# Kernel optimization log

Measured on AMD Instinct MI355X. Metric: run time of the kernel, lower is better.

The kernel has to match this reference:

```python
import jax, jax.numpy as jnp
import numpy as np

NUM_HEADS = 16
WINDOW = 256
DIM = 1024


def setup_inputs() -> dict:
    key = jax.random.key(0)
    k1, k2, k3, k4, k5 = jax.random.split(key, 5)
    B, L, D = 2, 2048, DIM
    s = 1.0 / np.sqrt(D)
    return {
        "x": jax.random.normal(k1, (B, L, D), dtype=jnp.float32),
        "in_proj_w": jax.random.uniform(k2, (3 * D, D), dtype=jnp.float32, minval=-s, maxval=s),
        "in_proj_b": jax.random.uniform(k3, (3 * D,), dtype=jnp.float32, minval=-s, maxval=s),
        "out_w": jax.random.uniform(k4, (D, D), dtype=jnp.float32, minval=-s, maxval=s),
        "out_b": jax.random.uniform(k5, (D,), dtype=jnp.float32, minval=-s, maxval=s),
    }


def reference(x, in_proj_w, in_proj_b, out_w, out_b):
    B, L, D = x.shape
    H = NUM_HEADS
    hd = D // H

    # combined qkv projection, as in nn.MultiheadAttention
    qkv = x @ in_proj_w.T + in_proj_b          # [B, L, 3D]
    q, k, v = jnp.split(qkv, 3, axis=-1)
    q = q.reshape(B, L, H, hd).transpose(0, 2, 1, 3)  # [B, H, L, hd]
    k = k.reshape(B, L, H, hd).transpose(0, 2, 1, 3)
    v = v.reshape(B, L, H, hd).transpose(0, 2, 1, 3)

    scale = 1.0 / jnp.sqrt(jnp.asarray(hd, dtype=x.dtype))
    scores = jnp.einsum("bhqd,bhkd->bhqk", q * scale, k)  # [B, H, L, L]

    # sliding-window causal mask: allowed iff i-window < j <= i
    i = jnp.arange(L)[:, None]
    j = jnp.arange(L)[None, :]
    allowed = (j <= i) & (j > i - WINDOW)                  # [L, L]
    scores = jnp.where(allowed[None, None], scores, -jnp.inf)

    attn = jax.nn.softmax(scores, axis=-1)
    out = jnp.einsum("bhqk,bhkd->bhqd", attn, v)           # [B, H, L, hd]
    out = out.transpose(0, 2, 1, 3).reshape(B, L, D)
    return out @ out_w.T + out_b
```

## Files before the change

### kernel.cpp

```cpp
#include <hip/hip_runtime.h>


#define SEQ_L 2048
#define WIN   256

typedef __bf16 bf16x8 __attribute__((ext_vector_type(8)));
typedef float  f32x4  __attribute__((ext_vector_type(4)));

__device__ __forceinline__ unsigned short f32_to_bf16(float f) {
  unsigned int u = __float_as_uint(f);
  u += 0x7FFFu + ((u >> 16) & 1u);
  return (unsigned short)(u >> 16);
}

__global__ void cast_kernel(const float* __restrict__ in,
                            unsigned short* __restrict__ out, int n4) {
  int i = blockIdx.x * 256 + threadIdx.x;
  if (i >= n4) return;
  float4 v = ((const float4*)in)[i];
  ushort4 o;
  o.x = f32_to_bf16(v.x); o.y = f32_to_bf16(v.y);
  o.z = f32_to_bf16(v.z); o.w = f32_to_bf16(v.w);
  ((ushort4*)out)[i] = o;
}

#define BK  64
#define LDK 72

template<int TBM, int TBN, int MI, int NI, int OUTBF>
__global__ __launch_bounds__(256) void gemm_nt(
    const unsigned short* __restrict__ A,
    const unsigned short* __restrict__ Bt,
    const float* __restrict__ bias,
    void* __restrict__ Cout, int M, int N, int K)
{
  __shared__ unsigned short As[TBM * LDK];
  __shared__ unsigned short Bs[TBN * LDK];

  const int tid  = threadIdx.x;
  const int lane = tid & 63;
  const int wave = tid >> 6;
  const int wr   = (wave >> 1) * (MI * 16);
  const int wc   = (wave & 1) * (NI * 16);
  const int quad = lane >> 4;
  const int l16  = lane & 15;

  const long m0 = (long)blockIdx.y * TBM;
  const long n0 = (long)blockIdx.x * TBN;

  f32x4 acc[MI][NI];
#pragma unroll
  for (int i = 0; i < MI; ++i)
#pragma unroll
    for (int j = 0; j < NI; ++j)
#pragma unroll
      for (int r = 0; r < 4; ++r) acc[i][j][r] = 0.0f;

  for (int k0 = 0; k0 < K; k0 += BK) {
#pragma unroll
    for (int p = 0; p < TBM / 32; ++p) {
      int c = p * 256 + tid, row = c >> 3, col8 = c & 7;
      *(uint4*)(&As[row * LDK + col8 * 8]) =
          *(const uint4*)(A + (m0 + row) * (long)K + k0 + col8 * 8);
    }
#pragma unroll
    for (int p = 0; p < TBN / 32; ++p) {
      int c = p * 256 + tid, row = c >> 3, col8 = c & 7;
      *(uint4*)(&Bs[row * LDK + col8 * 8]) =
          *(const uint4*)(Bt + (n0 + row) * (long)K + k0 + col8 * 8);
    }
    __syncthreads();
#pragma unroll
    for (int ks = 0; ks < 2; ++ks) {
      bf16x8 af[MI], bfv[NI];
#pragma unroll
      for (int mi = 0; mi < MI; ++mi)
        af[mi] = *(const bf16x8*)(&As[(wr + mi * 16 + l16) * LDK + ks * 32 + quad * 8]);
#pragma unroll
      for (int ni = 0; ni < NI; ++ni)
        bfv[ni] = *(const bf16x8*)(&Bs[(wc + ni * 16 + l16) * LDK + ks * 32 + quad * 8]);
#pragma unroll
      for (int mi = 0; mi < MI; ++mi)
#pragma unroll
        for (int ni = 0; ni < NI; ++ni)
          acc[mi][ni] = __builtin_amdgcn_mfma_f32_16x16x32_bf16(af[mi], bfv[ni], acc[mi][ni], 0, 0, 0);
    }
    __syncthreads();
  }

#pragma unroll
  for (int ni = 0; ni < NI; ++ni) {
    long col = n0 + wc + ni * 16 + l16;
    float bv = bias[col];
#pragma unroll
    for (int mi = 0; mi < MI; ++mi) {
      long rowb = m0 + wr + mi * 16 + quad * 4;
#pragma unroll
      for (int r = 0; r < 4; ++r) {
        float v = acc[mi][ni][r] + bv;
        if (OUTBF) ((unsigned short*)Cout)[(rowb + r) * N + col] = f32_to_bf16(v);
        else       ((float*)Cout)[(rowb + r) * N + col] = v;
      }
    }
  }
}

__global__ __launch_bounds__(256) void attn_kernel(
    const unsigned short* __restrict__ qkv,
    unsigned short* __restrict__ aout)
{
  __shared__ unsigned short Ks[64 * 72];
  __shared__ unsigned short Vt[64 * 72];
  __shared__ unsigned short Ps[4 * 16 * 72];

  const int tid  = threadIdx.x;
  const int w    = tid >> 6;
  const int lane = tid & 63;
  const int quad = lane >> 4;
  const int l16  = lane & 15;

  const int blk = blockIdx.x;
  const int qt  = blk & 31;
  const int h   = (blk >> 5) & 15;
  const int b   = blk >> 9;

  const int  i0  = qt * 64;
  const int  i0w = i0 + w * 16;
  const long rowbase = (long)b * SEQ_L;
  const float NEG_INF = -__builtin_inff();

  bf16x8 aq[2];
  {
    const unsigned short* qp = qkv + (rowbase + i0w + l16) * 3072 + h * 64 + quad * 8;
    aq[0] = *(const bf16x8*)(qp);
    aq[1] = *(const bf16x8*)(qp + 32);
  }

  f32x4 o[4];
#pragma unroll
  for (int ni = 0; ni < 4; ++ni)
#pragma unroll
    for (int r = 0; r < 4; ++r) o[ni][r] = 0.0f;
  float m_i[4], l_i[4];
#pragma unroll
  for (int r = 0; r < 4; ++r) { m_i[r] = NEG_INF; l_i[r] = 0.0f; }

  unsigned short* psw = &Ps[w * 16 * 72];

  const int j_begin = (i0 >= WIN) ? i0 - WIN : 0;

  for (int j0 = j_begin; j0 <= i0; j0 += 64) {
    __syncthreads();
#pragma unroll
    for (int p = 0; p < 2; ++p) {
      int c = p * 256 + tid, row = c >> 3, col8 = c & 7;
      const unsigned short* base = qkv + (rowbase + j0 + row) * 3072 + h * 64 + col8 * 8;
      *(uint4*)(&Ks[row * 72 + col8 * 8]) = *(const uint4*)(base + 1024);
      unsigned short tmp[8];
      *(uint4*)tmp = *(const uint4*)(base + 2048);
      int rsw = row ^ (col8 << 3);
#pragma unroll
      for (int e = 0; e < 8; ++e)
        Vt[(col8 * 8 + e) * 72 + rsw] = tmp[e];
    }
    __syncthreads();

    f32x4 s[4];
#pragma unroll
    for (int g = 0; g < 4; ++g) {
      bf16x8 k0 = *(const bf16x8*)(&Ks[(g * 16 + l16) * 72 + quad * 8]);
      bf16x8 k1 = *(const bf16x8*)(&Ks[(g * 16 + l16) * 72 + 32 + quad * 8]);
      f32x4 z;
#pragma unroll
      for (int r = 0; r < 4; ++r) z[r] = 0.0f;
      z = __builtin_amdgcn_mfma_f32_16x16x32_bf16(aq[0], k0, z, 0, 0, 0);
      z = __builtin_amdgcn_mfma_f32_16x16x32_bf16(aq[1], k1, z, 0, 0, 0);
      s[g] = z;
    }
#pragma unroll
    for (int g = 0; g < 4; ++g) {
      int j = j0 + g * 16 + l16;
#pragma unroll
      for (int r = 0; r < 4; ++r) {
        int i = i0w + quad * 4 + r;
        float sv = s[g][r] * 0.125f;
        bool ok = (j <= i) && (j > i - WIN);
        s[g][r] = ok ? sv : NEG_INF;
      }
    }
    float alpha[4];
#pragma unroll
    for (int r = 0; r < 4; ++r) {
      float mx = fmaxf(fmaxf(s[0][r], s[1][r]), fmaxf(s[2][r], s[3][r]));
      mx = fmaxf(mx, __shfl_xor(mx, 1));
      mx = fmaxf(mx, __shfl_xor(mx, 2));
      mx = fmaxf(mx, __shfl_xor(mx, 4));
      mx = fmaxf(mx, __shfl_xor(mx, 8));
      float m_new = fmaxf(m_i[r], mx);
      float a = (m_new == NEG_INF) ? 1.0f : __expf(m_i[r] - m_new);
      float rs = 0.0f;
#pragma unroll
      for (int g = 0; g < 4; ++g) {
        float e = (s[g][r] == NEG_INF) ? 0.0f : __expf(s[g][r] - m_new);
        psw[(quad * 4 + r) * 72 + g * 16 + l16] = f32_to_bf16(e);
        rs += e;
      }
      rs += __shfl_xor(rs, 1);
      rs += __shfl_xor(rs, 2);
      rs += __shfl_xor(rs, 4);
      rs += __shfl_xor(rs, 8);
      l_i[r] = l_i[r] * a + rs;
      m_i[r] = m_new;
      alpha[r] = a;
#pragma unroll
      for (int ni = 0; ni < 4; ++ni) o[ni][r] *= a;
    }
    asm volatile("s_waitcnt lgkmcnt(0)" ::: "memory");
#pragma unroll
    for (int kk = 0; kk < 2; ++kk) {
      bf16x8 ap = *(const bf16x8*)(&psw[l16 * 72 + kk * 32 + quad * 8]);
#pragma unroll
      for (int ni = 0; ni < 4; ++ni) {
        int d  = ni * 16 + l16;
        int rb = (kk * 32 + quad * 8) ^ (((d >> 3) & 7) << 3);
        bf16x8 bv = *(const bf16x8*)(&Vt[d * 72 + rb]);
        o[ni] = __builtin_amdgcn_mfma_f32_16x16x32_bf16(ap, bv, o[ni], 0, 0, 0);
      }
    }
  }

#pragma unroll
  for (int r = 0; r < 4; ++r) {
    float inv_l = 1.0f / l_i[r];
    long row = rowbase + i0w + quad * 4 + r;
#pragma unroll
    for (int ni = 0; ni < 4; ++ni)
      aout[row * 1024 + h * 64 + ni * 16 + l16] = f32_to_bf16(o[ni][r] * inv_l);
  }
}

extern "C" void kernel_launch(void* const* d_in, const int* in_sizes, int n_in,
                              void* d_out, int out_size, void* d_ws, size_t ws_size,
                              hipStream_t stream)
{
  const float* x  = (const float*)d_in[0];
  const float* w1 = (const float*)d_in[1];
  const float* b1 = (const float*)d_in[2];
  const float* w2 = (const float*)d_in[3];
  const float* b2 = (const float*)d_in[4];
  float* out = (float*)d_out;

  char* ws = (char*)d_ws;
  unsigned short* x_bf   = (unsigned short*)(ws);
  unsigned short* w1_bf  = (unsigned short*)(ws + 8388608);
  unsigned short* w2_bf  = (unsigned short*)(ws + 14680064);
  unsigned short* qkv_bf = (unsigned short*)(ws + 16777216);
  unsigned short* at_bf  = (unsigned short*)(ws + 41943040);

  cast_kernel<<<4096, 256, 0, stream>>>(x,  x_bf,  1048576);
  cast_kernel<<<3072, 256, 0, stream>>>(w1, w1_bf, 786432);
  cast_kernel<<<1024, 256, 0, stream>>>(w2, w2_bf, 262144);

  dim3 g1(3072 / 128, 4096 / 128);
  gemm_nt<128, 128, 4, 4, 1><<<g1, 256, 0, stream>>>(x_bf, w1_bf, b1, qkv_bf, 4096, 3072, 1024);

  attn_kernel<<<1024, 256, 0, stream>>>(qkv_bf, at_bf);

  dim3 g2(1024 / 64, 4096 / 128);
  gemm_nt<128, 64, 4, 2, 0><<<g2, 256, 0, stream>>>(at_bf, w2_bf, b2, out, 4096, 1024, 1024);
}
```

Measured before the change: 175.8 us.

## Load GEMM tiles with direct global-to-LDS copies and XOR-swizzled layout; merge casts

The GEMM now copies each A/B tile straight from global memory into LDS with global_load_lds. This skips the round trip through registers. LDS rows are unpadded, so an XOR swizzle on the 16-byte column chunk is used to avoid bank conflicts, and the fragment reads apply the same swizzle. The three fp32-to-bf16 cast launches are merged into one kernel to cut launch overhead. There is still no double buffering, so the async loads only remove the register staging; they do not overlap with compute.

```diff
diff --git a/kernel.cpp b/kernel.cpp
--- a/kernel.cpp
+++ b/kernel.cpp
@@ -13,19 +13,26 @@
   return (unsigned short)(u >> 16);
 }
 
-__global__ void cast_kernel(const float* __restrict__ in,
-                            unsigned short* __restrict__ out, int n4) {
+__device__ __forceinline__ void async16(const unsigned short* g, unsigned short* l) {
+  __builtin_amdgcn_global_load_lds(
+      (const __attribute__((address_space(1))) unsigned int*)g,
+      (__attribute__((address_space(3))) unsigned int*)l, 16, 0, 0);
+}
+
+__global__ void cast_all(const float* __restrict__ x,  unsigned short* __restrict__ xo,
+                         const float* __restrict__ w1, unsigned short* __restrict__ w1o,
+                         const float* __restrict__ w2, unsigned short* __restrict__ w2o) {
   int i = blockIdx.x * 256 + threadIdx.x;
-  if (i >= n4) return;
-  float4 v = ((const float4*)in)[i];
+  const float* in; unsigned short* out; int k;
+  if (i < 1048576)       { in = x;  out = xo;  k = i; }
+  else if (i < 1835008)  { in = w1; out = w1o; k = i - 1048576; }
+  else                   { in = w2; out = w2o; k = i - 1835008; }
+  float4 v = ((const float4*)in)[k];
   ushort4 o;
   o.x = f32_to_bf16(v.x); o.y = f32_to_bf16(v.y);
   o.z = f32_to_bf16(v.z); o.w = f32_to_bf16(v.w);
-  ((ushort4*)out)[i] = o;
-}
-
-#define BK  64
-#define LDK 72
+  ((ushort4*)out)[k] = o;
+}
 
 template<int TBM, int TBN, int MI, int NI, int OUTBF>
 __global__ __launch_bounds__(256) void gemm_nt(
@@ -34,8 +41,8 @@
     const float* __restrict__ bias,
     void* __restrict__ Cout, int M, int N, int K)
 {
-  __shared__ unsigned short As[TBM * LDK];
-  __shared__ unsigned short Bs[TBN * LDK];
+  __shared__ unsigned short As[TBM * 64];
+  __shared__ unsigned short Bs[TBN * 64];
 
   const int tid  = threadIdx.x;
   const int lane = tid & 63;
@@ -44,6 +51,8 @@
   const int wc   = (wave & 1) * (NI * 16);
   const int quad = lane >> 4;
   const int l16  = lane & 15;
+  const int lrow = lane >> 3;
+  const int scol = (lane & 7) ^ lrow;
 
   const long m0 = (long)blockIdx.y * TBM;
   const long n0 = (long)blockIdx.x * TBN;
@@ -56,29 +65,31 @@
 #pragma unroll
       for (int r = 0; r < 4; ++r) acc[i][j][r] = 0.0f;
 
-  for (int k0 = 0; k0 < K; k0 += BK) {
+  for (int k0 = 0; k0 < K; k0 += 64) {
 #pragma unroll
     for (int p = 0; p < TBM / 32; ++p) {
-      int c = p * 256 + tid, row = c >> 3, col8 = c & 7;
-      *(uint4*)(&As[row * LDK + col8 * 8]) =
-          *(const uint4*)(A + (m0 + row) * (long)K + k0 + col8 * 8);
+      int rb = wave * (TBM / 4) + p * 8;
+      async16(A + (m0 + rb + lrow) * (long)K + k0 + scol * 8, &As[rb * 64]);
     }
 #pragma unroll
     for (int p = 0; p < TBN / 32; ++p) {
-      int c = p * 256 + tid, row = c >> 3, col8 = c & 7;
-      *(uint4*)(&Bs[row * LDK + col8 * 8]) =
-          *(const uint4*)(Bt + (n0 + row) * (long)K + k0 + col8 * 8);
+      int rb = wave * (TBN / 4) + p * 8;
+      async16(Bt + (n0 + rb + lrow) * (long)K + k0 + scol * 8, &Bs[rb * 64]);
     }
     __syncthreads();
 #pragma unroll
     for (int ks = 0; ks < 2; ++ks) {
       bf16x8 af[MI], bfv[NI];
 #pragma unroll
-      for (int mi = 0; mi < MI; ++mi)
-        af[mi] = *(const bf16x8*)(&As[(wr + mi * 16 + l16) * LDK + ks * 32 + quad * 8]);
-#pragma unroll
-      for (int ni = 0; ni < NI; ++ni)
-        bfv[ni] = *(const bf16x8*)(&Bs[(wc + ni * 16 + l16) * LDK + ks * 32 + quad * 8]);
+      for (int mi = 0; mi < MI; ++mi) {
+        int r = wr + mi * 16 + l16;
+        af[mi] = *(const bf16x8*)(&As[r * 64 + ((ks * 4 + quad) ^ (r & 7)) * 8]);
+      }
+#pragma unroll
+      for (int ni = 0; ni < NI; ++ni) {
+        int r = wc + ni * 16 + l16;
+        bfv[ni] = *(const bf16x8*)(&Bs[r * 64 + ((ks * 4 + quad) ^ (r & 7)) * 8]);
+      }
 #pragma unroll
       for (int mi = 0; mi < MI; ++mi)
 #pragma unroll
@@ -257,9 +268,7 @@
   unsigned short* qkv_bf = (unsigned short*)(ws + 16777216);
   unsigned short* at_bf  = (unsigned short*)(ws + 41943040);
 
-  cast_kernel<<<4096, 256, 0, stream>>>(x,  x_bf,  1048576);
-  cast_kernel<<<3072, 256, 0, stream>>>(w1, w1_bf, 786432);
-  cast_kernel<<<1024, 256, 0, stream>>>(w2, w2_bf, 262144);
+  cast_all<<<8192, 256, 0, stream>>>(x, x_bf, w1, w1_bf, w2, w2_bf);
 
   dim3 g1(3072 / 128, 4096 / 128);
   gemm_nt<128, 128, 4, 4, 1><<<g1, 256, 0, stream>>>(x_bf, w1_bf, b1, qkv_bf, 4096, 3072, 1024);
```

After: 170.0 us. 1.03x faster.
